# Kernel tuning notes

Measured on AMD Instinct MI355X. Metric: run time of the kernel, lower is better.

Reference implementation:

```python
import jax, jax.numpy as jnp
import numpy as np
from itertools import combinations

DILATIONS = [1, 2, 4, 8]
NUM_KERNELS = 84  # C(9,3)
KERNEL_LEN = 9


def setup_inputs() -> dict:
    key = jax.random.key(0)
    k_x, k_mask, k_bias, k_mean, k_std = jax.random.split(key, 5)
    B, L, C = 64, 2048, 8
    D = len(DILATIONS)
    F = 4  # features (biases) per kernel per dilation
    num_features = D * NUM_KERNELS * F

    # MiniRocket fixed kernels: -1 everywhere, +2 at each 3-index combination
    idx = np.asarray(list(combinations(range(KERNEL_LEN), 3)), dtype=np.int64)
    base = np.full((NUM_KERNELS, KERNEL_LEN), -1.0, dtype=np.float32)
    for i in range(NUM_KERNELS):
        base[i, idx[i]] = 2.0

    x = jax.random.normal(k_x, (B, L, C), dtype=jnp.float32)
    # binary channel masks per (dilation, kernel): which channels contribute
    channel_masks = (jax.random.uniform(k_mask, (D, NUM_KERNELS, C)) < 0.5).astype(jnp.float32)
    bias_matrices = jax.random.normal(k_bias, (D, NUM_KERNELS, F), dtype=jnp.float32)
    feature_mean = jax.random.normal(k_mean, (num_features,), dtype=jnp.float32)
    feature_std = jax.random.uniform(k_std, (num_features,), minval=0.5, maxval=1.5, dtype=jnp.float32)
    return {
        "x": x,
        "kernels": jnp.asarray(base),
        "channel_masks": channel_masks,
        "bias_matrices": bias_matrices,
        "feature_mean": feature_mean,
        "feature_std": feature_std,
    }


def _extract(x, kernels, channel_masks, bias_matrices):
    B, L, C = x.shape
    D, K, F = bias_matrices.shape
    x_cf = jnp.transpose(x, (0, 2, 1))  # [B, C, L]
    dtype = x.dtype
    t = jnp.arange(L)
    feats_all = []
    for d_idx, dil in enumerate(DILATIONS):
        pad = (KERNEL_LEN - 1) * dil // 2  # = 4*dil, so conv output length == L
        # Since the depthwise kernel is identical across channels for a given
        # kernel index, masked-channel-sum commutes with the conv:
        # response[b,k,:] = conv(sum_c mask[k,c] * x[b,c,:], kernel_k)
        mixed = jnp.einsum('kc,bcl->bkl', channel_masks[d_idx], x_cf)  # [B,K,L]
        resp = jax.lax.conv_general_dilated(
            mixed, kernels[:, None, :],
            window_strides=(1,), padding=[(pad, pad)],
            rhs_dilation=(dil,),
            dimension_numbers=('NCH', 'OIH', 'NCH'),
            feature_group_count=K,
        )  # [B, K, L]
        # PPV time-weights: kernels with odd (dilation_index + kernel_index)
        # are trimmed to the interior [pad, L-pad); others use the full length.
        should_trim = (pad > 0) and (L - 2 * pad > 0)
        interior = ((t >= pad) & (t < L - pad)).astype(dtype)  # [L]
        w_full = jnp.full((L,), 1.0 / L, dtype=dtype)
        w_trim = interior / jnp.asarray(L - 2 * pad, dtype=dtype)
        parity_odd = ((d_idx + jnp.arange(K)) % 2 == 1) & should_trim  # [K]
        w = jnp.where(parity_odd[:, None], w_trim[None, :], w_full[None, :])  # [K,L]
        # PPV: fraction of timesteps where response exceeds each bias
        ind = (resp[:, :, None, :] > bias_matrices[d_idx][None, :, :, None]).astype(dtype)  # [B,K,F,L]
        feats = jnp.einsum('bkfl,kl->bkf', ind, w)  # [B,K,F]
        feats_all.append(feats.reshape(B, K * F))
    return jnp.concatenate(feats_all, axis=1)  # [B, D*K*F]


def reference(x, kernels, channel_masks, bias_matrices, feature_mean, feature_std):
    flat = _extract(x, kernels, channel_masks, bias_matrices)
    return (flat - feature_mean) / feature_std
```

## Files before the change

kernel.cpp:

```cpp
#include <hip/hip_runtime.h>

#define TL 2048
#define TC 8
#define TK 84
#define TF 4
#define TD 4
#define ROWS 352
#define NFEAT (TD * TK * TF)
#define KF (TK * TF)
#define NQ 8

typedef unsigned int u32;
typedef __fp16 hf8 __attribute__((ext_vector_type(8)));
typedef float f32x4 __attribute__((ext_vector_type(4)));

__device__ __forceinline__ u32 pkrtz(float a, float b) {
    return __builtin_bit_cast(u32, __builtin_amdgcn_cvt_pkrtz(a, b));
}
__device__ __forceinline__ int swzrow(int e) { return e ^ ((e >> 3) & 7); }

__device__ __forceinline__ u32 red16(u32 v) {
    v += (u32)__builtin_amdgcn_update_dpp(0, (int)v, 0xB1,  0xF, 0xF, true);
    v += (u32)__builtin_amdgcn_update_dpp(0, (int)v, 0x4E,  0xF, 0xF, true);
    v += (u32)__builtin_amdgcn_update_dpp(0, (int)v, 0x141, 0xF, 0xF, true);
    v += (u32)__builtin_amdgcn_update_dpp(0, (int)v, 0x140, 0xF, 0xF, true);
    return v;
}

__global__ __launch_bounds__(256, 4) void mr_main(
    const float* __restrict__ x,
    const float* __restrict__ kern,
    const float* __restrict__ cmask,
    const float* __restrict__ bias,
    int* __restrict__ ws)
{
    __shared__ __align__(16) uint4 xh[ROWS];
    __shared__ __align__(16) uint4 Alds[1152];
    __shared__ __align__(16) float4 blds[TK];
    __shared__ u32 feats2[6][4][16];

    const int bx = blockIdx.x;
    const int q = bx & 7, d = (bx >> 3) & 3, b = bx >> 5;
    const int tid = threadIdx.x, lane = tid & 63, w = tid >> 6;
    const int dil = 1 << d, pad = 4 << d;
    const int t0 = q * 256;
    const float* xb = x + (size_t)b * TL * TC;

    if (tid < TK) blds[tid] = *(const float4*)(bias + ((size_t)d * TK + tid) * TF);

    for (int f = tid; f < 1152; f += 256) {
        const int col = f & 15, lg = (f >> 4) & 3, kbkt = f >> 6;
        const int kt = kbkt / 3, kb = kbkt % 3;
        const int k = kt * 16 + col, j = kb * 4 + lg;
        uint4 v = {0u, 0u, 0u, 0u};
        if (k < TK && j < 9) {
            const float wv = kern[k * 9 + j];
            const float* mp = cmask + ((size_t)d * TK + k) * TC;
            const float4 m0 = *(const float4*)mp;
            const float4 m1 = *(const float4*)(mp + 4);
            v.x = pkrtz(m0.x != 0.f ? wv : 0.f, m0.y != 0.f ? wv : 0.f);
            v.y = pkrtz(m0.z != 0.f ? wv : 0.f, m0.w != 0.f ? wv : 0.f);
            v.z = pkrtz(m1.x != 0.f ? wv : 0.f, m1.y != 0.f ? wv : 0.f);
            v.w = pkrtz(m1.z != 0.f ? wv : 0.f, m1.w != 0.f ? wv : 0.f);
        }
        Alds[f] = v;
    }

    for (int e = tid; e < ROWS; e += 256) {
        const int pos = t0 - 32 + e;
        uint4 v = {0u, 0u, 0u, 0u};
        if (pos >= 0 && pos < TL) {
            const float4* xp = (const float4*)(xb + (size_t)pos * TC);
            const float4 a = xp[0], h = xp[1];
            v.x = pkrtz(a.x, a.y); v.y = pkrtz(a.z, a.w);
            v.z = pkrtz(h.x, h.y); v.w = pkrtz(h.z, h.w);
        }
        xh[swzrow(e)] = v;
    }
    __syncthreads();

    const int col = lane & 15, lg = lane >> 4;

    hf8 bf[12];
    #pragma unroll
    for (int i = 0; i < 4; ++i)
        #pragma unroll
        for (int kb = 0; kb < 3; ++kb) {
            const int e = 32 + col - 4 * dil + (w * 4 + i) * 16 + (kb * 4 + lg) * dil;
            bf[i * 3 + kb] = __builtin_bit_cast(hf8, xh[swzrow(e)]);
        }

    bool interior[4];
    #pragma unroll
    for (int i = 0; i < 4; ++i) {
        const int tfirst = t0 + (w * 4 + i) * 16;
        interior[i] = (tfirst >= pad) && (tfirst + 16 <= TL - pad);
    }

    for (int kt = 0; kt < 6; ++kt) {
        hf8 af[3];
        #pragma unroll
        for (int kb = 0; kb < 3; ++kb)
            af[kb] = __builtin_bit_cast(hf8, Alds[(kt * 3 + kb) * 64 + lane]);

        float4 bq[4];
        #pragma unroll
        for (int rg = 0; rg < 4; ++rg) {
            int k = kt * 16 + lg * 4 + rg;
            k = (k < TK) ? k : (TK - 1);
            bq[rg] = blds[k];
        }

        u32 cnt[4] = {0u, 0u, 0u, 0u};

        #pragma unroll
        for (int i = 0; i < 4; ++i) {
            f32x4 C = {0.f, 0.f, 0.f, 0.f};
            #pragma unroll
            for (int kb = 0; kb < 3; ++kb)
                C = __builtin_amdgcn_mfma_f32_16x16x32_f16(af[kb], bf[i * 3 + kb], C, 0, 0, 0);

            if (interior[i]) {
                #pragma unroll
                for (int rg = 0; rg < 4; ++rg) {
                    const float cv = C[rg];
                    cnt[rg] += (cv > bq[rg].x) ? 0x1u : 0u;
                    cnt[rg] += (cv > bq[rg].y) ? 0x100u : 0u;
                    cnt[rg] += (cv > bq[rg].z) ? 0x10000u : 0u;
                    cnt[rg] += (cv > bq[rg].w) ? 0x1000000u : 0u;
                }
            } else {
                const int t = t0 + (w * 4 + i) * 16 + col;
                const bool ok = (t >= pad && t < TL - pad);
                #pragma unroll
                for (int rg = 0; rg < 4; ++rg) {
                    const float cv = C[rg];
                    const bool use = ((d ^ rg) & 1) ? ok : true;
                    cnt[rg] += (use && cv > bq[rg].x) ? 0x1u : 0u;
                    cnt[rg] += (use && cv > bq[rg].y) ? 0x100u : 0u;
                    cnt[rg] += (use && cv > bq[rg].z) ? 0x10000u : 0u;
                    cnt[rg] += (use && cv > bq[rg].w) ? 0x1000000u : 0u;
                }
            }
        }

        #pragma unroll
        for (int rg = 0; rg < 4; ++rg) cnt[rg] = red16(cnt[rg]);

        if (col == 0) {
            #pragma unroll
            for (int rg = 0; rg < 4; ++rg)
                feats2[kt][w][lg * 4 + rg] = cnt[rg];
        }
    }

    __syncthreads();
    for (int idx = tid; idx < KF; idx += 256) {
        const int k = idx >> 2, f = idx & 3;
        const int kt = k >> 4, r = k & 15;
        int cnt = 0;
        #pragma unroll
        for (int wv = 0; wv < 4; ++wv)
            cnt += (int)((feats2[kt][wv][r] >> (8 * f)) & 0xFFu);
        ws[(size_t)bx * KF + idx] = cnt;
    }
}

__global__ void mr_fin(const int* __restrict__ ws, const float* __restrict__ fmean,
                       const float* __restrict__ fstd, float* __restrict__ out) {
    const int o = blockIdx.x * 256 + threadIdx.x;
    const int fid = o % NFEAT, b = o / NFEAT;
    const int d = fid / KF, idx = fid % KF, k = idx >> 2;
    const int base = ((b * 32 + d * 8) * KF) + idx;
    int cnt = 0;
    #pragma unroll
    for (int q = 0; q < NQ; ++q) cnt += ws[base + q * KF];
    const float denom = ((d + k) & 1) ? (float)(TL - (8 << d)) : (float)TL;
    out[o] = ((float)cnt / denom - fmean[fid]) / fstd[fid];
}

extern "C" void kernel_launch(void* const* d_in, const int* in_sizes, int n_in,
                              void* d_out, int out_size, void* d_ws, size_t ws_size,
                              hipStream_t stream) {
    const float* x     = (const float*)d_in[0];
    const float* kern  = (const float*)d_in[1];
    const float* cmask = (const float*)d_in[2];
    const float* bias  = (const float*)d_in[3];
    const float* fmean = (const float*)d_in[4];
    const float* fstd  = (const float*)d_in[5];
    float* out = (float*)d_out;
    int* ws = (int*)d_ws;

    hipLaunchKernelGGL(mr_main, dim3(64 * TD * NQ), dim3(256), 0, stream,
                       x, kern, cmask, bias, ws);
    hipLaunchKernelGGL(mr_fin, dim3(64 * NFEAT / 256), dim3(256), 0, stream,
                       ws, fmean, fstd, out);
}
```

Before: 33.84 us.

## Precompute masked kernel fragments in a prep kernel and read them from global

Adds a small mr_prep kernel that builds the masked fp16 A-operand fragments once per dilation into workspace, instead of every block rebuilding them into LDS. The main kernel drops the 18KB Alds buffer, reads A fragments directly from global/L2, and loads B fragments from LDS inside the MFMA loop rather than keeping 12 in registers. Launch bounds go from 4 to 8 waves per SIMD target, aiming at higher occupancy. The cost is an extra kernel launch, global-memory latency on the A loads in the inner loop, and more LDS reads per MFMA.

```diff
diff --git a/kernel.cpp b/kernel.cpp
--- a/kernel.cpp
+++ b/kernel.cpp
@@ -27,15 +27,35 @@
     return v;
 }
 
-__global__ __launch_bounds__(256, 4) void mr_main(
+__global__ void mr_prep(const float* __restrict__ kern, const float* __restrict__ cmask,
+                        uint4* __restrict__ A) {
+    const int idx = blockIdx.x * 256 + threadIdx.x;
+    if (idx >= TD * 18 * 64) return;
+    const int lane = idx & 63, kbkt = (idx >> 6) % 18, d = idx / (18 * 64);
+    const int kt = kbkt / 3, kb = kbkt % 3;
+    const int col = lane & 15, lg = lane >> 4;
+    const int k = kt * 16 + col, j = kb * 4 + lg;
+    uint4 v = {0u, 0u, 0u, 0u};
+    if (k < TK && j < 9) {
+        const float wv = kern[k * 9 + j];
+        const float* mp = cmask + ((size_t)d * TK + k) * TC;
+        const float4 m0 = *(const float4*)mp;
+        const float4 m1 = *(const float4*)(mp + 4);
+        v.x = pkrtz(m0.x != 0.f ? wv : 0.f, m0.y != 0.f ? wv : 0.f);
+        v.y = pkrtz(m0.z != 0.f ? wv : 0.f, m0.w != 0.f ? wv : 0.f);
+        v.z = pkrtz(m1.x != 0.f ? wv : 0.f, m1.y != 0.f ? wv : 0.f);
+        v.w = pkrtz(m1.z != 0.f ? wv : 0.f, m1.w != 0.f ? wv : 0.f);
+    }
+    A[idx] = v;
+}
+
+__global__ __launch_bounds__(256, 8) void mr_main(
     const float* __restrict__ x,
-    const float* __restrict__ kern,
-    const float* __restrict__ cmask,
+    const uint4* __restrict__ A,
     const float* __restrict__ bias,
     int* __restrict__ ws)
 {
     __shared__ __align__(16) uint4 xh[ROWS];
-    __shared__ __align__(16) uint4 Alds[1152];
     __shared__ __align__(16) float4 blds[TK];
     __shared__ u32 feats2[6][4][16];
 
@@ -47,24 +67,6 @@
     const float* xb = x + (size_t)b * TL * TC;
 
     if (tid < TK) blds[tid] = *(const float4*)(bias + ((size_t)d * TK + tid) * TF);
-
-    for (int f = tid; f < 1152; f += 256) {
-        const int col = f & 15, lg = (f >> 4) & 3, kbkt = f >> 6;
-        const int kt = kbkt / 3, kb = kbkt % 3;
-        const int k = kt * 16 + col, j = kb * 4 + lg;
-        uint4 v = {0u, 0u, 0u, 0u};
-        if (k < TK && j < 9) {
-            const float wv = kern[k * 9 + j];
-            const float* mp = cmask + ((size_t)d * TK + k) * TC;
-            const float4 m0 = *(const float4*)mp;
-            const float4 m1 = *(const float4*)(mp + 4);
-            v.x = pkrtz(m0.x != 0.f ? wv : 0.f, m0.y != 0.f ? wv : 0.f);
-            v.y = pkrtz(m0.z != 0.f ? wv : 0.f, m0.w != 0.f ? wv : 0.f);
-            v.z = pkrtz(m1.x != 0.f ? wv : 0.f, m1.y != 0.f ? wv : 0.f);
-            v.w = pkrtz(m1.z != 0.f ? wv : 0.f, m1.w != 0.f ? wv : 0.f);
-        }
-        Alds[f] = v;
-    }
 
     for (int e = tid; e < ROWS; e += 256) {
         const int pos = t0 - 32 + e;
@@ -80,14 +82,15 @@
     __syncthreads();
 
     const int col = lane & 15, lg = lane >> 4;
-
-    hf8 bf[12];
+    const uint4* Ad = A + d * 18 * 64;
+
+    int addrs[12];
     #pragma unroll
     for (int i = 0; i < 4; ++i)
         #pragma unroll
         for (int kb = 0; kb < 3; ++kb) {
             const int e = 32 + col - 4 * dil + (w * 4 + i) * 16 + (kb * 4 + lg) * dil;
-            bf[i * 3 + kb] = __builtin_bit_cast(hf8, xh[swzrow(e)]);
+            addrs[i * 3 + kb] = swzrow(e) * 16;
         }
 
     bool interior[4];
@@ -101,7 +104,7 @@
         hf8 af[3];
         #pragma unroll
         for (int kb = 0; kb < 3; ++kb)
-            af[kb] = __builtin_bit_cast(hf8, Alds[(kt * 3 + kb) * 64 + lane]);
+            af[kb] = __builtin_bit_cast(hf8, Ad[(kt * 3 + kb) * 64 + lane]);
 
         float4 bq[4];
         #pragma unroll
@@ -117,8 +120,10 @@
         for (int i = 0; i < 4; ++i) {
             f32x4 C = {0.f, 0.f, 0.f, 0.f};
             #pragma unroll
-            for (int kb = 0; kb < 3; ++kb)
-                C = __builtin_amdgcn_mfma_f32_16x16x32_f16(af[kb], bf[i * 3 + kb], C, 0, 0, 0);
+            for (int kb = 0; kb < 3; ++kb) {
+                const hf8 bf = *(const hf8*)((const char*)xh + addrs[i * 3 + kb]);
+                C = __builtin_amdgcn_mfma_f32_16x16x32_f16(af[kb], bf, C, 0, 0, 0);
+            }
 
             if (interior[i]) {
                 #pragma unroll
@@ -189,10 +194,14 @@
     const float* fmean = (const float*)d_in[4];
     const float* fstd  = (const float*)d_in[5];
     float* out = (float*)d_out;
-    int* ws = (int*)d_ws;
-
+
+    uint4* Aws = (uint4*)d_ws;
+    int* cws = (int*)((char*)d_ws + TD * 18 * 64 * 16);
+
+    hipLaunchKernelGGL(mr_prep, dim3((TD * 18 * 64 + 255) / 256), dim3(256), 0, stream,
+                       kern, cmask, Aws);
     hipLaunchKernelGGL(mr_main, dim3(64 * TD * NQ), dim3(256), 0, stream,
-                       x, kern, cmask, bias, ws);
+                       x, Aws, bias, cws);
     hipLaunchKernelGGL(mr_fin, dim3(64 * NFEAT / 256), dim3(256), 0, stream,
-                       ws, fmean, fstd, out);
-}
+                       cws, fmean, fstd, out);
+}
```

Result: slower. 88.73 us (+162.2%).
